# Performance work log

Measured on AMD Instinct MI355X. Metric: run time of the kernel, lower is better.

Reference implementation:

```python
import jax, jax.numpy as jnp
import numpy as np
from jax import lax

DIM = 384
HEADS = 8

def setup_inputs() -> dict:
    key = jax.random.key(0)
    ks = jax.random.split(key, 7)
    B, C, H, W = 4, DIM, 128, 128
    x = jax.random.normal(ks[0], (B, C, H, W), dtype=jnp.float32)
    y = jax.random.normal(ks[1], (B, C, H, W), dtype=jnp.float32)
    s1 = 1.0 / np.sqrt(C)
    Wq = jax.random.normal(ks[2], (C, C), dtype=jnp.float32) * s1          # 1x1 conv [out,in]
    Wkv = jax.random.normal(ks[3], (2 * C, C), dtype=jnp.float32) * s1     # 1x1 conv
    Wdw = jax.random.normal(ks[4], (3 * C, 1, 3, 3), dtype=jnp.float32) * (1.0 / 3.0)  # depthwise 3x3
    Wproj = jax.random.normal(ks[5], (C, C), dtype=jnp.float32) * s1       # 1x1 conv
    temperature = jnp.ones((HEADS, 1, 1), dtype=jnp.float32)
    return {"x": x, "y": y, "Wq": Wq, "Wkv": Wkv, "Wdw": Wdw,
            "Wproj": Wproj, "temperature": temperature}


def _conv1x1(x, W):
    # x: [b,c,h,w], W: [o,c] -> [b,o,h,w]
    return jnp.einsum('bchw,oc->bohw', x, W)


def _l2norm(t, eps=1e-12):
    n = jnp.sqrt(jnp.sum(t * t, axis=-1, keepdims=True))
    return t / jnp.maximum(n, eps)


def reference(x, y, Wq, Wkv, Wdw, Wproj, temperature):
    b, c, h, w = x.shape
    q = _conv1x1(x, Wq)                     # [b,c,h,w]
    kv = _conv1x1(y, Wkv)                   # [b,2c,h,w]
    qkv = jnp.concatenate([q, kv], axis=1)  # [b,3c,h,w]
    qkv = lax.conv_general_dilated(
        qkv, Wdw, window_strides=(1, 1), padding='SAME',
        dimension_numbers=('NCHW', 'OIHW', 'NCHW'),
        feature_group_count=3 * c)
    q, k, v = jnp.split(qkv, 3, axis=1)
    cp = c // HEADS
    hw = h * w
    # b (head c) h w -> b head c (h w)
    q = q.reshape(b, HEADS, cp, hw)
    k = k.reshape(b, HEADS, cp, hw)
    v = v.reshape(b, HEADS, cp, hw)
    q = _l2norm(q)
    k = _l2norm(k)
    attn = jnp.einsum('bhcn,bhdn->bhcd', q, k) * temperature  # [b,head,cp,cp]
    attn = jax.nn.softmax(attn, axis=-1)
    out = jnp.einsum('bhcd,bhdn->bhcn', attn, v)              # [b,head,cp,hw]
    out = out.reshape(b, c, h, w)
    return _conv1x1(out, Wproj)
```

## Files before the change

kernel.cpp:

```cpp
#include <hip/hip_runtime.h>
#include <hip/hip_bf16.h>

#define DIM 384
#define HEADS 8
#define CP 48
#define NB 4
#define HIMG 128
#define WIMG 128
#define HW 16384

using bf16 = __hip_bfloat16;

typedef __attribute__((ext_vector_type(8))) short bf16x8;
typedef __attribute__((ext_vector_type(4))) float f32x4;

__device__ __forceinline__ float lo_bf(unsigned u){ union{unsigned i; float f;} c; c.i = u<<16; return c.f; }
__device__ __forceinline__ float hi_bf(unsigned u){ union{unsigned i; float f;} c; c.i = u & 0xffff0000u; return c.f; }
__device__ __forceinline__ bf16 f2bf(float v){ return __float2bfloat16(v); }
__device__ __forceinline__ unsigned short bfbits(float v){ union{ bf16 h; unsigned short u; } c; c.h = f2bf(v); return c.u; }

__device__ __forceinline__ float4 load4f(const float* p){ return *(const float4*)p; }
__device__ __forceinline__ float4 load4f(const bf16* p){
  uint2 u = *(const uint2*)p;
  float4 r; r.x = lo_bf(u.x); r.y = hi_bf(u.x); r.z = lo_bf(u.y); r.w = hi_bf(u.y); return r;
}

__device__ __forceinline__ void st(float* p, float v){ *p = v; }
__device__ __forceinline__ void st(bf16* p, float v){ *p = f2bf(v); }

#define GLD_LDS16(g, l) __builtin_amdgcn_global_load_lds( \
    (const __attribute__((address_space(1))) void*)(g), \
    (__attribute__((address_space(3))) void*)(l), 16, 0, 0)

__global__ __launch_bounds__(256) void convert_w(
    const float* __restrict__ Wq, const float* __restrict__ Wkv,
    bf16* __restrict__ Wq_bf, bf16* __restrict__ Wkv_bf)
{
  int idx = (blockIdx.x*256 + threadIdx.x) * 2;
  const int NQ = DIM*DIM;
  const int NKV = 2*DIM*DIM;
  if (idx < NQ) {
    unsigned u = (unsigned)bfbits(Wq[idx]) | ((unsigned)bfbits(Wq[idx+1]) << 16);
    *(unsigned*)(Wq_bf + idx) = u;
  } else {
    int j = idx - NQ;
    if (j < NKV) {
      unsigned u = (unsigned)bfbits(Wkv[j]) | ((unsigned)bfbits(Wkv[j+1]) << 16);
      *(unsigned*)(Wkv_bf + j) = u;
    }
  }
}

template<typename TIn>
__global__ __launch_bounds__(256) void transpose_cast(
    const TIn* __restrict__ in0, const TIn* __restrict__ in1,
    bf16* __restrict__ out0, bf16* __restrict__ out1,
    long inBatchStride, long outBatchStride)
{
  const int zb = blockIdx.z;
  const TIn* in = (zb < NB) ? in0 : in1;
  bf16* outp = (zb < NB) ? out0 : out1;
  const int b = zb & 3;
  const int n0 = blockIdx.x * 64;
  const int c0 = blockIdx.y * 64;
  const TIn* inb = in + (long)b * inBatchStride;
  bf16* outb = outp + (long)b * outBatchStride;

  __shared__ float tile[64][66];
  const int t = threadIdx.x;
#pragma unroll
  for (int i = 0; i < 4; ++i) {
    int g = i*256 + t;
    int r = g >> 4, c4 = g & 15;
    float4 v = load4f(inb + (long)(c0 + r)*HW + n0 + c4*4);
    tile[r][c4*4+0] = v.x; tile[r][c4*4+1] = v.y;
    tile[r][c4*4+2] = v.z; tile[r][c4*4+3] = v.w;
  }
  __syncthreads();
#pragma unroll
  for (int i = 0; i < 8; ++i) {
    int g = i*256 + t;
    int n = g >> 5, cu = g & 31;
    unsigned u = (unsigned)bfbits(tile[cu*2][n]) | ((unsigned)bfbits(tile[cu*2+1][n]) << 16);
    *(unsigned*)(outb + (long)(n0 + n)*DIM + c0 + cu*2) = u;
  }
}

template<typename TOut>
__global__ __launch_bounds__(256) void gemm_mfma(
    const bf16* __restrict__ A, long aStride,
    const bf16* __restrict__ Bt, TOut* __restrict__ C, int M, int K)
{
  const int b  = blockIdx.z;
  const int m0 = blockIdx.y * 128;
  const int n0 = blockIdx.x * 128;
  const bf16* Ab  = A  + (long)b * aStride;
  const bf16* Btb = Bt + (long)b * (long)HW * K;
  TOut* Cb = C + (long)b * (long)M * HW;

  __shared__ short As[128*64];
  __shared__ short Bs[128*64];

  const int t = threadIdx.x;
  const int w = t >> 6, lane = t & 63;
  const int quad = lane >> 4, l16 = lane & 15;
  const int wm = (w >> 1) * 64, wn = (w & 1) * 64;

  const bf16* gA[4]; const bf16* gB[4];
#pragma unroll
  for (int i = 0; i < 4; ++i) {
    int f = w*256 + i*64 + lane;
    int r = f >> 3, p = f & 7;
    int c = p ^ (r & 7);
    gA[i] = Ab  + (long)(m0 + r)*K + c*8;
    gB[i] = Btb + (long)(n0 + r)*K + c*8;
  }

  f32x4 acc[4][4] = {};

  for (int k0 = 0; k0 < K; k0 += 64) {
#pragma unroll
    for (int i = 0; i < 4; ++i) {
      GLD_LDS16(gA[i], As + (w*256 + i*64)*8);
      GLD_LDS16(gB[i], Bs + (w*256 + i*64)*8);
      gA[i] += 64; gB[i] += 64;
    }
    __syncthreads();
#pragma unroll
    for (int kk = 0; kk < 2; ++kk) {
      bf16x8 af[4], bfr[4];
      const int sw = (kk*4 + quad) ^ (l16 & 7);
#pragma unroll
      for (int mt = 0; mt < 4; ++mt) {
        af[mt]  = *(const bf16x8*)(As + (wm + mt*16 + l16)*64 + sw*8);
        bfr[mt] = *(const bf16x8*)(Bs + (wn + mt*16 + l16)*64 + sw*8);
      }
#pragma unroll
      for (int mt = 0; mt < 4; ++mt)
#pragma unroll
        for (int nt = 0; nt < 4; ++nt)
          acc[mt][nt] = __builtin_amdgcn_mfma_f32_16x16x32_bf16(af[mt], bfr[nt], acc[mt][nt], 0, 0, 0);
    }
    __syncthreads();
  }

#pragma unroll
  for (int mt = 0; mt < 4; ++mt)
#pragma unroll
    for (int nt = 0; nt < 4; ++nt)
#pragma unroll
      for (int j = 0; j < 4; ++j) {
        int row = m0 + wm + mt*16 + quad*4 + j;
        int col = n0 + wn + nt*16 + l16;
        st(Cb + (long)row*HW + col, acc[mt][nt][j]);
      }
}

__global__ __launch_bounds__(256) void dwconv_inplace(
    bf16* __restrict__ qb, bf16* __restrict__ kvb,
    const float* __restrict__ Wdw, float* __restrict__ ssq)
{
  const int ch = blockIdx.x;
  const int b  = blockIdx.y;
  bf16* plane = (ch < DIM) ? qb + ((long)b*DIM + ch)*HW
                           : kvb + ((long)b*2*DIM + (ch - DIM))*HW;
  float w9[9];
#pragma unroll
  for (int i = 0; i < 9; ++i) w9[i] = Wdw[ch*9 + i];

  __shared__ bf16 t_[128*140];
  const int t = threadIdx.x;
#pragma unroll
  for (int i = 0; i < 16; ++i) {
    int g = i*256 + t;
    int r = g >> 5, c4 = g & 31;
    *(uint2*)&t_[r*140 + c4*4] = *(const uint2*)(plane + r*128 + c4*4);
  }
  __syncthreads();

  const int r = t >> 1, half = t & 1, cbase = half*64;
  const float mtop = (r > 0)   ? 1.f : 0.f;
  const float mbot = (r < 127) ? 1.f : 0.f;
  const int rt = (r > 0)   ? r-1 : r;
  const int rb = (r < 127) ? r+1 : r;

  float a0,a1,a2,b0,b1,b2,c0,c1,c2;
#define LD3(cc, A, B, Cv) { A = __bfloat162float(t_[rt*140 + (cc)]) * mtop; \
                            B = __bfloat162float(t_[r*140 + (cc)]); \
                            Cv = __bfloat162float(t_[rb*140 + (cc)]) * mbot; }
  if (cbase == 0) { a0=b0=c0=0.f; } else LD3(cbase-1, a0, b0, c0);
  LD3(cbase,   a1, b1, c1);
  LD3(cbase+1, a2, b2, c2);

  float ss = 0.f;
  unsigned outu[32];
#pragma unroll 4
  for (int j = 0; j < 64; ++j) {
    float o = w9[0]*a0 + w9[1]*a1 + w9[2]*a2
            + w9[3]*b0 + w9[4]*b1 + w9[5]*b2
            + w9[6]*c0 + w9[7]*c1 + w9[8]*c2;
    ss += o*o;
    unsigned short ob = bfbits(o);
    if (j & 1) outu[j>>1] |= ((unsigned)ob << 16); else outu[j>>1] = ob;
    a0=a1; a1=a2; b0=b1; b1=b2; c0=c1; c1=c2;
    int nc = cbase + j + 2;
    if (nc <= 127) { LD3(nc, a2, b2, c2) } else { a2=b2=c2=0.f; }
  }
#undef LD3

#pragma unroll
  for (int i = 0; i < 8; ++i)
    *(uint4*)(plane + r*128 + cbase + i*8) = *(uint4*)&outu[i*4];

  if (ch < 2*DIM) {
#pragma unroll
    for (int off = 32; off; off >>= 1) ss += __shfl_down(ss, off);
    __shared__ float wsum[4];
    if ((t & 63) == 0) wsum[t >> 6] = ss;
    __syncthreads();
    if (t == 0) ssq[b*2*DIM + ch] = wsum[0]+wsum[1]+wsum[2]+wsum[3];
  }
}

__global__ __launch_bounds__(512) void s_mfma(
    const bf16* __restrict__ qd, const bf16* __restrict__ kd,
    float* __restrict__ Sp)
{
  const int split = blockIdx.x;
  const int h = blockIdx.y, b = blockIdx.z;
  const int t = threadIdx.x, w = t >> 6, lane = t & 63;
  const int quad = lane >> 4, l16 = lane & 15;
  const bf16* qp = qd + ((long)b*DIM + h*CP)*HW;
  const bf16* kp = kd + ((long)b*DIM + h*CP)*HW;
  const int nbase = (split*8 + w) * 256;

  f32x4 acc[3][3] = {};
  for (int ks = 0; ks < 8; ++ks) {
    const int n = nbase + ks*32 + quad*8;
    bf16x8 aq[3], bk[3];
#pragma unroll
    for (int i = 0; i < 3; ++i) {
      aq[i] = *(const bf16x8*)(qp + (long)(i*16 + l16)*HW + n);
      bk[i] = *(const bf16x8*)(kp + (long)(i*16 + l16)*HW + n);
    }
#pragma unroll
    for (int i = 0; i < 3; ++i)
#pragma unroll
      for (int j = 0; j < 3; ++j)
        acc[i][j] = __builtin_amdgcn_mfma_f32_16x16x32_bf16(aq[i], bk[j], acc[i][j], 0, 0, 0);
  }

  __shared__ float Sred[8][CP*CP];
#pragma unroll
  for (int i = 0; i < 3; ++i)
#pragma unroll
    for (int j = 0; j < 3; ++j)
#pragma unroll
      for (int rr = 0; rr < 4; ++rr)
        Sred[w][(i*16 + quad*4 + rr)*CP + j*16 + l16] = acc[i][j][rr];
  __syncthreads();

  float* out = Sp + (long)split*(NB*HEADS*CP*CP) + ((long)(b*HEADS + h))*CP*CP;
  for (int g = t; g < CP*CP; g += 512) {
    float s = 0.f;
#pragma unroll
    for (int ww = 0; ww < 8; ++ww) s += Sred[ww][g];
    out[g] = s;
  }
}

__global__ __launch_bounds__(64) void softmax_attn(
    float* __restrict__ Sp, const float* __restrict__ ssq,
    const float* __restrict__ temp)
{
  const int bhc = blockIdx.x;
  const int c = bhc % CP;
  const int h = (bhc / CP) % HEADS;
  const int b = bhc / (CP * HEADS);
  const int lane = threadIdx.x;
  const long rowoff = ((long)(b*HEADS + h))*CP*CP + c*CP;
  const float rq = rsqrtf(ssq[b*2*DIM + h*CP + c]);
  const float tmp = temp[h];
  float logit = -1e30f;
  if (lane < CP) {
    float s = 0.f;
#pragma unroll
    for (int sl = 0; sl < 8; ++sl) s += Sp[(long)sl*(NB*HEADS*CP*CP) + rowoff + lane];
    float rk = rsqrtf(ssq[b*2*DIM + DIM + h*CP + lane]);
    logit = s * rq * rk * tmp;
  }
  float m = logit;
#pragma unroll
  for (int off = 32; off; off >>= 1) m = fmaxf(m, __shfl_down(m, off));
  m = __shfl(m, 0);
  float e = (lane < CP) ? __expf(logit - m) : 0.f;
  float s = e;
#pragma unroll
  for (int off = 32; off; off >>= 1) s += __shfl_down(s, off);
  s = __shfl(s, 0);
  if (lane < CP) Sp[rowoff + lane] = e / s;
}

__global__ __launch_bounds__(256) void w2fold(
    const float* __restrict__ attn, const float* __restrict__ Wproj,
    bf16* __restrict__ W2)
{
  const int ot = blockIdx.x;
  const int h  = blockIdx.y;
  const int b  = blockIdx.z;
  __shared__ float at[CP][CP];
  __shared__ float wp[128][CP];
  const int t = threadIdx.x;
  const float* Ap = attn + ((long)(b*HEADS + h))*CP*CP;
#pragma unroll
  for (int i = 0; i < 9; ++i) {
    int idx = t + 256*i;
    at[idx / CP][idx % CP] = Ap[idx];
  }
#pragma unroll
  for (int i = 0; i < 24; ++i) {
    int idx = t + 256*i;
    int o = idx / CP, c = idx % CP;
    wp[o][c] = Wproj[(long)(ot*128 + o)*DIM + h*CP + c];
  }
  __syncthreads();
#pragma unroll
  for (int i = 0; i < 24; ++i) {
    int idx = t + 256*i;
    int o = idx / CP, d = idx % CP;
    float a = 0.f;
#pragma unroll
    for (int c = 0; c < CP; ++c) a += wp[o][c] * at[c][d];
    W2[((long)b*DIM + ot*128 + o)*DIM + h*CP + d] = f2bf(a);
  }
}

extern "C" void kernel_launch(void* const* d_in, const int* in_sizes, int n_in,
                              void* d_out, int out_size, void* d_ws, size_t ws_size,
                              hipStream_t stream) {
  const float* x     = (const float*)d_in[0];
  const float* y     = (const float*)d_in[1];
  const float* Wq    = (const float*)d_in[2];
  const float* Wkv   = (const float*)d_in[3];
  const float* Wdw   = (const float*)d_in[4];
  const float* Wproj = (const float*)d_in[5];
  const float* temp  = (const float*)d_in[6];
  float* out = (float*)d_out;

  char* ws = (char*)d_ws;
  const long SZ_T  = 50331648L;
  bf16* xT    = (bf16*)(ws + 0L);
  bf16* yT    = (bf16*)(ws + SZ_T);
  bf16* q_bf  = (bf16*)(ws + 2*SZ_T);
  bf16* kv_bf = (bf16*)(ws + 3*SZ_T);
  char* tail  = ws + 5*SZ_T;
  bf16* Wq_bf  = (bf16*)(tail);
  bf16* Wkv_bf = (bf16*)(tail + 294912L);
  float* Sp    = (float*)(tail);
  bf16* W2_bf  = (bf16*)(tail + 294912L);
  float* ssq   = (float*)(tail + 2359296L);
  bf16* vdT    = xT;
  bf16* vd     = kv_bf + (long)DIM*HW;

  convert_w<<<864, 256, 0, stream>>>(Wq, Wkv, Wq_bf, Wkv_bf);
  transpose_cast<float><<<dim3(HW/64, DIM/64, 8), 256, 0, stream>>>(
      x, y, xT, yT, (long)DIM*HW, (long)HW*DIM);
  gemm_mfma<bf16><<<dim3(HW/128, DIM/128, NB), 256, 0, stream>>>(
      Wq_bf, 0, xT, q_bf, DIM, DIM);
  gemm_mfma<bf16><<<dim3(HW/128, 2*DIM/128, NB), 256, 0, stream>>>(
      Wkv_bf, 0, yT, kv_bf, 2*DIM, DIM);
  dwconv_inplace<<<dim3(3*DIM, NB), 256, 0, stream>>>(q_bf, kv_bf, Wdw, ssq);
  transpose_cast<bf16><<<dim3(HW/64, DIM/64, NB), 256, 0, stream>>>(
      vd, nullptr, vdT, nullptr, (long)2*DIM*HW, (long)HW*DIM);
  s_mfma<<<dim3(8, HEADS, NB), 512, 0, stream>>>(q_bf, kv_bf, Sp);
  softmax_attn<<<dim3(NB*HEADS*CP), 64, 0, stream>>>(Sp, ssq, temp);
  w2fold<<<dim3(3, HEADS, NB), 256, 0, stream>>>(Sp, Wproj, W2_bf);
  gemm_mfma<float><<<dim3(HW/128, DIM/128, NB), 256, 0, stream>>>(
      W2_bf, (long)DIM*DIM, vdT, out, DIM, DIM);
}
```

Baseline: 558.2 us.

## Process depthwise conv in two half-plane passes with smaller LDS and coalesced stores

The depthwise 3x3 conv kernel now stages 66 rows (64 plus halo) in LDS instead of the full 128-row plane, processing the plane in two halves. The shared-memory footprint shrinks so more blocks can be resident, and launch bounds request 6 blocks per CU. Each thread computes 32 outputs with vectorised 4-wide bf16 loads, stages results back through LDS, and writes rows with coalesced 16-byte stores. In exchange there are extra barriers and a second load phase for the halo and lower half.

```diff
diff --git a/kernel.cpp b/kernel.cpp
--- a/kernel.cpp
+++ b/kernel.cpp
@@ -18,6 +18,11 @@
 __device__ __forceinline__ float hi_bf(unsigned u){ union{unsigned i; float f;} c; c.i = u & 0xffff0000u; return c.f; }
 __device__ __forceinline__ bf16 f2bf(float v){ return __float2bfloat16(v); }
 __device__ __forceinline__ unsigned short bfbits(float v){ union{ bf16 h; unsigned short u; } c; c.h = f2bf(v); return c.u; }
+__device__ __forceinline__ float s2f(short s){ union{unsigned u; float f;} c; c.u = ((unsigned)(unsigned short)s) << 16; return c.f; }
+__device__ __forceinline__ void cvt4(const short* p, float* o){
+  uint2 u = *(const uint2*)p;
+  o[0]=lo_bf(u.x); o[1]=hi_bf(u.x); o[2]=lo_bf(u.y); o[3]=hi_bf(u.y);
+}
 
 __device__ __forceinline__ float4 load4f(const float* p){ return *(const float4*)p; }
 __device__ __forceinline__ float4 load4f(const bf16* p){
@@ -156,7 +161,7 @@
       }
 }
 
-__global__ __launch_bounds__(256) void dwconv_inplace(
+__global__ __launch_bounds__(256, 6) void dwconv_inplace(
     bf16* __restrict__ qb, bf16* __restrict__ kvb,
     const float* __restrict__ Wdw, float* __restrict__ ssq)
 {
@@ -168,54 +173,116 @@
 #pragma unroll
   for (int i = 0; i < 9; ++i) w9[i] = Wdw[ch*9 + i];
 
-  __shared__ bf16 t_[128*140];
+  __shared__ short t_[66*140];
+  __shared__ float wsum[4];
   const int t = threadIdx.x;
-#pragma unroll
-  for (int i = 0; i < 16; ++i) {
-    int g = i*256 + t;
-    int r = g >> 5, c4 = g & 31;
-    *(uint2*)&t_[r*140 + c4*4] = *(const uint2*)(plane + r*128 + c4*4);
-  }
-  __syncthreads();
-
-  const int r = t >> 1, half = t & 1, cbase = half*64;
-  const float mtop = (r > 0)   ? 1.f : 0.f;
-  const float mbot = (r < 127) ? 1.f : 0.f;
-  const int rt = (r > 0)   ? r-1 : r;
-  const int rb = (r < 127) ? r+1 : r;
-
-  float a0,a1,a2,b0,b1,b2,c0,c1,c2;
-#define LD3(cc, A, B, Cv) { A = __bfloat162float(t_[rt*140 + (cc)]) * mtop; \
-                            B = __bfloat162float(t_[r*140 + (cc)]); \
-                            Cv = __bfloat162float(t_[rb*140 + (cc)]) * mbot; }
-  if (cbase == 0) { a0=b0=c0=0.f; } else LD3(cbase-1, a0, b0, c0);
-  LD3(cbase,   a1, b1, c1);
-  LD3(cbase+1, a2, b2, c2);
-
+
+  if (t < 66) *(uint2*)&t_[t*140 + 128] = make_uint2(0u, 0u);
+
+#pragma unroll
+  for (int i = 0; i < 9; ++i) {
+    int chunk = i*256 + t;
+    if (chunk < 66*32) {
+      int r = chunk >> 5, c8 = chunk & 31;
+      int gh = r - 1;
+      uint2 v = make_uint2(0u, 0u);
+      if (gh >= 0) v = *(const uint2*)(plane + gh*128 + c8*4);
+      *(uint2*)&t_[r*140 + c8*4] = v;
+    }
+  }
+  __syncthreads();
+
+  const int r  = t >> 2;
+  const int q  = t & 3;
+  const int c0 = q * 32;
   float ss = 0.f;
-  unsigned outu[32];
-#pragma unroll 4
-  for (int j = 0; j < 64; ++j) {
-    float o = w9[0]*a0 + w9[1]*a1 + w9[2]*a2
-            + w9[3]*b0 + w9[4]*b1 + w9[5]*b2
-            + w9[6]*c0 + w9[7]*c1 + w9[8]*c2;
-    ss += o*o;
-    unsigned short ob = bfbits(o);
-    if (j & 1) outu[j>>1] |= ((unsigned)ob << 16); else outu[j>>1] = ob;
-    a0=a1; a1=a2; b0=b1; b1=b2; c0=c1; c1=c2;
-    int nc = cbase + j + 2;
-    if (nc <= 127) { LD3(nc, a2, b2, c2) } else { a2=b2=c2=0.f; }
-  }
-#undef LD3
-
-#pragma unroll
-  for (int i = 0; i < 8; ++i)
-    *(uint4*)(plane + r*128 + cbase + i*8) = *(uint4*)&outu[i*4];
+  unsigned outu[16];
+
+  auto compute = [&]() {
+    const short* rT = t_ + (r    )*140 + c0;
+    const short* rM = t_ + (r + 1)*140 + c0;
+    const short* rB = t_ + (r + 2)*140 + c0;
+    float at[4], am[4], ab[4];
+    cvt4(rT, at); cvt4(rM, am); cvt4(rB, ab);
+    float lt, lm, lb;
+    if (q == 0) { lt = lm = lb = 0.f; }
+    else { lt = s2f(rT[-1]); lm = s2f(rM[-1]); lb = s2f(rB[-1]); }
+#pragma unroll
+    for (int jb = 0; jb < 32; jb += 4) {
+      float bt[4], bm[4], bb[4];
+      cvt4(rT + jb + 4, bt);
+      cvt4(rM + jb + 4, bm);
+      cvt4(rB + jb + 4, bb);
+      float o0 = w9[0]*lt    + w9[1]*at[0] + w9[2]*at[1]
+               + w9[3]*lm    + w9[4]*am[0] + w9[5]*am[1]
+               + w9[6]*lb    + w9[7]*ab[0] + w9[8]*ab[1];
+      float o1 = w9[0]*at[0] + w9[1]*at[1] + w9[2]*at[2]
+               + w9[3]*am[0] + w9[4]*am[1] + w9[5]*am[2]
+               + w9[6]*ab[0] + w9[7]*ab[1] + w9[8]*ab[2];
+      float o2 = w9[0]*at[1] + w9[1]*at[2] + w9[2]*at[3]
+               + w9[3]*am[1] + w9[4]*am[2] + w9[5]*am[3]
+               + w9[6]*ab[1] + w9[7]*ab[2] + w9[8]*ab[3];
+      float o3 = w9[0]*at[2] + w9[1]*at[3] + w9[2]*bt[0]
+               + w9[3]*am[2] + w9[4]*am[3] + w9[5]*bm[0]
+               + w9[6]*ab[2] + w9[7]*ab[3] + w9[8]*bb[0];
+      ss += o0*o0 + o1*o1 + o2*o2 + o3*o3;
+      outu[(jb>>1)  ] = (unsigned)bfbits(o0) | ((unsigned)bfbits(o1) << 16);
+      outu[(jb>>1)+1] = (unsigned)bfbits(o2) | ((unsigned)bfbits(o3) << 16);
+      lt = at[3]; lm = am[3]; lb = ab[3];
+#pragma unroll
+      for (int u2 = 0; u2 < 4; ++u2) { at[u2]=bt[u2]; am[u2]=bm[u2]; ab[u2]=bb[u2]; }
+    }
+  };
+
+  compute();
+  uint2 halo = make_uint2(0u, 0u);
+  if (t < 64) halo = *(const uint2*)&t_[(64 + (t >> 5))*140 + (t & 31)*4];
+  __syncthreads();
+
+#pragma unroll
+  for (int i2 = 0; i2 < 8; ++i2)
+    *(uint2*)&t_[r*140 + c0 + i2*4] = *(uint2*)&outu[i2*2];
+  __syncthreads();
+#pragma unroll
+  for (int i2 = 0; i2 < 4; ++i2) {
+    int chunk = i2*256 + t;
+    int orow = chunk >> 4, ocol = (chunk & 15)*8;
+    uint2 lo = *(const uint2*)&t_[orow*140 + ocol];
+    uint2 hi = *(const uint2*)&t_[orow*140 + ocol + 4];
+    *(uint4*)(plane + (long)orow*128 + ocol) = make_uint4(lo.x, lo.y, hi.x, hi.y);
+  }
+  __syncthreads();
+
+  if (t < 64) *(uint2*)&t_[(t >> 5)*140 + (t & 31)*4] = halo;
+#pragma unroll
+  for (int i2 = 0; i2 < 8; ++i2) {
+    int chunk = i2*256 + t;
+    int rr = chunk >> 5, c8 = chunk & 31;
+    int gh = 65 + rr;
+    uint2 v = make_uint2(0u, 0u);
+    if (gh < 128) v = *(const uint2*)(plane + gh*128 + c8*4);
+    *(uint2*)&t_[(rr + 2)*140 + c8*4] = v;
+  }
+  __syncthreads();
+
+  compute();
+  __syncthreads();
+#pragma unroll
+  for (int i2 = 0; i2 < 8; ++i2)
+    *(uint2*)&t_[r*140 + c0 + i2*4] = *(uint2*)&outu[i2*2];
+  __syncthreads();
+#pragma unroll
+  for (int i2 = 0; i2 < 4; ++i2) {
+    int chunk = i2*256 + t;
+    int orow = chunk >> 4, ocol = (chunk & 15)*8;
+    uint2 lo = *(const uint2*)&t_[orow*140 + ocol];
+    uint2 hi = *(const uint2*)&t_[orow*140 + ocol + 4];
+    *(uint4*)(plane + (long)(64 + orow)*128 + ocol) = make_uint4(lo.x, lo.y, hi.x, hi.y);
+  }
 
   if (ch < 2*DIM) {
 #pragma unroll
     for (int off = 32; off; off >>= 1) ss += __shfl_down(ss, off);
-    __shared__ float wsum[4];
     if ((t & 63) == 0) wsum[t >> 6] = ss;
     __syncthreads();
     if (t == 0) ssq[b*2*DIM + ch] = wsum[0]+wsum[1]+wsum[2]+wsum[3];
```

Result: no change. 568.3 us (+1.8%).
